# Optimization experiments

Measured on AMD Instinct MI355X. Metric: run time of the kernel, lower is better.

Reference implementation:

```python
import jax, jax.numpy as jnp
import numpy as np

N_NODES = 65536
NUM_GRAPHS = 128
NODES_PER_GRAPH = N_NODES // NUM_GRAPHS
HIDDEN = 512
EPS = 1e-6


def setup_inputs() -> dict:
    key = jax.random.key(0)
    k1, = jax.random.split(key, 1)
    x = jax.random.normal(k1, (N_NODES, HIDDEN), dtype=jnp.float32)
    gnw = jnp.ones((HIDDEN,), dtype=jnp.float32)
    gnb = jnp.zeros((HIDDEN,), dtype=jnp.float32)
    msc = jnp.ones((HIDDEN,), dtype=jnp.float32)
    batch_num = jnp.full((NUM_GRAPHS,), NODES_PER_GRAPH, dtype=jnp.int64)
    return {"x": x, "gnw": gnw, "gnb": gnb, "msc": msc, "batch_num": batch_num}


def reference(x, gnw, gnb, msc, batch_num):
    # x: [N, D] node features; batch_num: [B] per-graph node counts (sum == N)
    B = batch_num.shape[0]
    N = x.shape[0]
    seg = jnp.repeat(jnp.arange(B), batch_num, total_repeat_length=N)  # [N] graph id per node
    counts = batch_num.astype(x.dtype)[:, None]  # [B, 1]
    # per-graph mean: scatter-add then divide by segment size
    mean = jax.ops.segment_sum(x, seg, num_segments=B) / counts  # [B, D]
    sub = x - mean[seg] * msc  # [N, D]
    # per-graph variance of `sub` (matches original: second scatter_add of sub^2)
    var = jax.ops.segment_sum(sub * sub, seg, num_segments=B) / counts  # [B, D]
    std = jnp.sqrt(var + EPS)  # [B, D]
    return gnw * sub / std[seg] + gnb
```

## Files before the change

### kernel.cpp

```cpp
#include <hip/hip_runtime.h>


constexpr int N_NODES    = 65536;
constexpr int NUM_GRAPHS = 128;
constexpr int NPG        = N_NODES / NUM_GRAPHS;
constexpr int D          = 512;
constexpr int D4         = D / 4;
constexpr int RG         = 8;
constexpr int ROWS_PER_T = NPG / RG;
constexpr float EPS      = 1e-6f;

__global__ __launch_bounds__(1024) void k_graphnorm(const float* __restrict__ x,
                                                    const float* __restrict__ gnw,
                                                    const float* __restrict__ gnb,
                                                    const float* __restrict__ msc,
                                                    float* __restrict__ out) {
    __shared__ float4 lsum[RG][D4];
    __shared__ float4 lsq [RG][D4];
    __shared__ float4 lA[D4], lB[D4];

    const int g   = blockIdx.x;
    const int tid = threadIdx.x;
    const int cq  = tid & (D4 - 1);
    const int rg  = tid >> 7;

    const float4* xg = reinterpret_cast<const float4*>(x) + (size_t)g * NPG * D4;
    float4*       og = reinterpret_cast<float4*>(out)     + (size_t)g * NPG * D4;

    float4 s = make_float4(0.f, 0.f, 0.f, 0.f);
    float4 q = make_float4(0.f, 0.f, 0.f, 0.f);
    #pragma unroll 8
    for (int i = 0; i < ROWS_PER_T; ++i) {
        const int r = rg + i * RG;
        float4 v = xg[(size_t)r * D4 + cq];
        s.x += v.x; s.y += v.y; s.z += v.z; s.w += v.w;
        q.x = fmaf(v.x, v.x, q.x);
        q.y = fmaf(v.y, v.y, q.y);
        q.z = fmaf(v.z, v.z, q.z);
        q.w = fmaf(v.w, v.w, q.w);
    }
    lsum[rg][cq] = s;
    lsq [rg][cq] = q;
    __syncthreads();

    if (tid < D4) {
        const int d = tid;
        float4 S1 = lsum[0][d], S2 = lsq[0][d];
        #pragma unroll
        for (int j = 1; j < RG; ++j) {
            float4 a = lsum[j][d], b = lsq[j][d];
            S1.x += a.x; S1.y += a.y; S1.z += a.z; S1.w += a.w;
            S2.x += b.x; S2.y += b.y; S2.z += b.z; S2.w += b.w;
        }
        const float inv_n = 1.0f / (float)NPG;
        const float4 w4 = reinterpret_cast<const float4*>(gnw)[d];
        const float4 b4 = reinterpret_cast<const float4*>(gnb)[d];
        const float4 m4 = reinterpret_cast<const float4*>(msc)[d];
        float4 A, B;
        {
            float m, c, var, rstd;
            m = S1.x * inv_n; c = m * m4.x;
            var = fmaxf(fmaf(c, c, fmaf(-2.f * c, m, S2.x * inv_n)), 0.f);
            rstd = rsqrtf(var + EPS); A.x = w4.x * rstd; B.x = fmaf(-A.x, c, b4.x);
            m = S1.y * inv_n; c = m * m4.y;
            var = fmaxf(fmaf(c, c, fmaf(-2.f * c, m, S2.y * inv_n)), 0.f);
            rstd = rsqrtf(var + EPS); A.y = w4.y * rstd; B.y = fmaf(-A.y, c, b4.y);
            m = S1.z * inv_n; c = m * m4.z;
            var = fmaxf(fmaf(c, c, fmaf(-2.f * c, m, S2.z * inv_n)), 0.f);
            rstd = rsqrtf(var + EPS); A.z = w4.z * rstd; B.z = fmaf(-A.z, c, b4.z);
            m = S1.w * inv_n; c = m * m4.w;
            var = fmaxf(fmaf(c, c, fmaf(-2.f * c, m, S2.w * inv_n)), 0.f);
            rstd = rsqrtf(var + EPS); A.w = w4.w * rstd; B.w = fmaf(-A.w, c, b4.w);
        }
        lA[d] = A;
        lB[d] = B;
    }
    __syncthreads();

    const float4 a = lA[cq];
    const float4 b = lB[cq];
    #pragma unroll 8
    for (int i = 0; i < ROWS_PER_T; ++i) {
        const size_t o = (size_t)(rg + i * RG) * D4 + cq;
        float4 v = xg[o];
        float4 r;
        r.x = fmaf(a.x, v.x, b.x);
        r.y = fmaf(a.y, v.y, b.y);
        r.z = fmaf(a.z, v.z, b.z);
        r.w = fmaf(a.w, v.w, b.w);
        og[o] = r;
    }
}

extern "C" void kernel_launch(void* const* d_in, const int* in_sizes, int n_in,
                              void* d_out, int out_size, void* d_ws, size_t ws_size,
                              hipStream_t stream) {
    const float* x   = (const float*)d_in[0];
    const float* gnw = (const float*)d_in[1];
    const float* gnb = (const float*)d_in[2];
    const float* msc = (const float*)d_in[3];
    float* out = (float*)d_out;

    k_graphnorm<<<NUM_GRAPHS, 1024, 0, stream>>>(x, gnw, gnb, msc, out);
}
```

Baseline: 253.1 us.

## Split graph norm into stats, finalize, and normalize kernels across more blocks

Replaces the single kernel, which ran one 1024-thread block per graph (128 blocks), with three kernels. A partial-stats kernel over 2048 blocks writes per-slice sums to workspace, a small finalize kernel reduces them into per-graph scale/shift, and a normalize kernel over 2048 blocks applies them with nontemporal stores. The aim is to fill all CUs, since 128 blocks underuse a 256-CU GPU. In exchange it adds two extra launches and a workspace round trip, and x is still read twice.

```diff
diff --git a/kernel.cpp b/kernel.cpp
--- a/kernel.cpp
+++ b/kernel.cpp
@@ -1,94 +1,112 @@
 #include <hip/hip_runtime.h>
 
 
-constexpr int N_NODES    = 65536;
+using f32x4 = __attribute__((ext_vector_type(4))) float;
+
 constexpr int NUM_GRAPHS = 128;
-constexpr int NPG        = N_NODES / NUM_GRAPHS;
+constexpr int NPG        = 512;
 constexpr int D          = 512;
 constexpr int D4         = D / 4;
-constexpr int RG         = 8;
-constexpr int ROWS_PER_T = NPG / RG;
+constexpr int SLICES     = 16;
+constexpr int ROWS_PS    = NPG / SLICES;
+constexpr int RG         = 2;
+constexpr int ROWS_PT    = ROWS_PS / RG;
 constexpr float EPS      = 1e-6f;
 
-__global__ __launch_bounds__(1024) void k_graphnorm(const float* __restrict__ x,
-                                                    const float* __restrict__ gnw,
-                                                    const float* __restrict__ gnb,
-                                                    const float* __restrict__ msc,
-                                                    float* __restrict__ out) {
-    __shared__ float4 lsum[RG][D4];
-    __shared__ float4 lsq [RG][D4];
-    __shared__ float4 lA[D4], lB[D4];
 
-    const int g   = blockIdx.x;
-    const int tid = threadIdx.x;
-    const int cq  = tid & (D4 - 1);
-    const int rg  = tid >> 7;
+__global__ __launch_bounds__(256) void k_stats(const float* __restrict__ x,
+                                               f32x4* __restrict__ part) {
+    const int b  = blockIdx.x;
+    const int cq = threadIdx.x & (D4 - 1);
+    const int rg = threadIdx.x >> 7;
 
-    const float4* xg = reinterpret_cast<const float4*>(x) + (size_t)g * NPG * D4;
-    float4*       og = reinterpret_cast<float4*>(out)     + (size_t)g * NPG * D4;
+    const f32x4* xp = reinterpret_cast<const f32x4*>(x)
+                    + (size_t)b * ROWS_PS * D4 + (size_t)rg * D4 + cq;
 
-    float4 s = make_float4(0.f, 0.f, 0.f, 0.f);
-    float4 q = make_float4(0.f, 0.f, 0.f, 0.f);
-    #pragma unroll 8
-    for (int i = 0; i < ROWS_PER_T; ++i) {
-        const int r = rg + i * RG;
-        float4 v = xg[(size_t)r * D4 + cq];
-        s.x += v.x; s.y += v.y; s.z += v.z; s.w += v.w;
-        q.x = fmaf(v.x, v.x, q.x);
-        q.y = fmaf(v.y, v.y, q.y);
-        q.z = fmaf(v.z, v.z, q.z);
-        q.w = fmaf(v.w, v.w, q.w);
+    f32x4 s = {0.f, 0.f, 0.f, 0.f};
+    f32x4 q = {0.f, 0.f, 0.f, 0.f};
+    #pragma unroll
+    for (int i = 0; i < ROWS_PT; ++i) {
+        f32x4 v = xp[(size_t)i * RG * D4];
+        s += v;
+        q += v * v;
     }
-    lsum[rg][cq] = s;
-    lsq [rg][cq] = q;
-    __syncthreads();
 
-    if (tid < D4) {
-        const int d = tid;
-        float4 S1 = lsum[0][d], S2 = lsq[0][d];
+    f32x4* p = part + (((size_t)b * RG + rg) * 2) * D4 + cq;
+    p[0]  = s;
+    p[D4] = q;
+}
+
+__device__ inline float2 finalize1(float s1, float s2, float w, float bi,
+                                   float ms) {
+    const float inv_n = 1.0f / (float)NPG;
+    const float m = s1 * inv_n;
+    const float c = m * ms;
+    float var = fmaxf(fmaf(c, c, fmaf(-2.f * c, m, s2 * inv_n)), 0.f);
+    const float r = rsqrtf(var + EPS);
+    const float A = w * r;
+    const float B = fmaf(-A, c, bi);
+    return make_float2(A, B);
+}
+
+__global__ __launch_bounds__(256) void k_finalize(const f32x4* __restrict__ part,
+                                                  const float* __restrict__ gnw,
+                                                  const float* __restrict__ gnb,
+                                                  const float* __restrict__ msc,
+                                                  f32x4* __restrict__ Aa,
+                                                  f32x4* __restrict__ Ba) {
+    const int idx = blockIdx.x * 256 + threadIdx.x;
+    const int g   = idx >> 7;
+    const int cq  = idx & (D4 - 1);
+
+    f32x4 S1 = {0.f, 0.f, 0.f, 0.f};
+    f32x4 S2 = {0.f, 0.f, 0.f, 0.f};
+    #pragma unroll
+    for (int sl = 0; sl < SLICES; ++sl) {
         #pragma unroll
-        for (int j = 1; j < RG; ++j) {
-            float4 a = lsum[j][d], b = lsq[j][d];
-            S1.x += a.x; S1.y += a.y; S1.z += a.z; S1.w += a.w;
-            S2.x += b.x; S2.y += b.y; S2.z += b.z; S2.w += b.w;
+        for (int rg = 0; rg < RG; ++rg) {
+            const f32x4* p = part
+                + (((size_t)(g * SLICES + sl) * RG + rg) * 2) * D4 + cq;
+            S1 += p[0];
+            S2 += p[D4];
         }
-        const float inv_n = 1.0f / (float)NPG;
-        const float4 w4 = reinterpret_cast<const float4*>(gnw)[d];
-        const float4 b4 = reinterpret_cast<const float4*>(gnb)[d];
-        const float4 m4 = reinterpret_cast<const float4*>(msc)[d];
-        float4 A, B;
-        {
-            float m, c, var, rstd;
-            m = S1.x * inv_n; c = m * m4.x;
-            var = fmaxf(fmaf(c, c, fmaf(-2.f * c, m, S2.x * inv_n)), 0.f);
-            rstd = rsqrtf(var + EPS); A.x = w4.x * rstd; B.x = fmaf(-A.x, c, b4.x);
-            m = S1.y * inv_n; c = m * m4.y;
-            var = fmaxf(fmaf(c, c, fmaf(-2.f * c, m, S2.y * inv_n)), 0.f);
-            rstd = rsqrtf(var + EPS); A.y = w4.y * rstd; B.y = fmaf(-A.y, c, b4.y);
-            m = S1.z * inv_n; c = m * m4.z;
-            var = fmaxf(fmaf(c, c, fmaf(-2.f * c, m, S2.z * inv_n)), 0.f);
-            rstd = rsqrtf(var + EPS); A.z = w4.z * rstd; B.z = fmaf(-A.z, c, b4.z);
-            m = S1.w * inv_n; c = m * m4.w;
-            var = fmaxf(fmaf(c, c, fmaf(-2.f * c, m, S2.w * inv_n)), 0.f);
-            rstd = rsqrtf(var + EPS); A.w = w4.w * rstd; B.w = fmaf(-A.w, c, b4.w);
-        }
-        lA[d] = A;
-        lB[d] = B;
     }
-    __syncthreads();
 
-    const float4 a = lA[cq];
-    const float4 b = lB[cq];
-    #pragma unroll 8
-    for (int i = 0; i < ROWS_PER_T; ++i) {
-        const size_t o = (size_t)(rg + i * RG) * D4 + cq;
-        float4 v = xg[o];
-        float4 r;
-        r.x = fmaf(a.x, v.x, b.x);
-        r.y = fmaf(a.y, v.y, b.y);
-        r.z = fmaf(a.z, v.z, b.z);
-        r.w = fmaf(a.w, v.w, b.w);
-        og[o] = r;
+    const f32x4 w4 = reinterpret_cast<const f32x4*>(gnw)[cq];
+    const f32x4 b4 = reinterpret_cast<const f32x4*>(gnb)[cq];
+    const f32x4 m4 = reinterpret_cast<const f32x4*>(msc)[cq];
+    f32x4 A, B;
+    float2 r;
+    r = finalize1(S1.x, S2.x, w4.x, b4.x, m4.x); A.x = r.x; B.x = r.y;
+    r = finalize1(S1.y, S2.y, w4.y, b4.y, m4.y); A.y = r.x; B.y = r.y;
+    r = finalize1(S1.z, S2.z, w4.z, b4.z, m4.z); A.z = r.x; B.z = r.y;
+    r = finalize1(S1.w, S2.w, w4.w, b4.w, m4.w); A.w = r.x; B.w = r.y;
+
+    Aa[(size_t)g * D4 + cq] = A;
+    Ba[(size_t)g * D4 + cq] = B;
+}
+
+__global__ __launch_bounds__(256) void k_norm(const float* __restrict__ x,
+                                              const f32x4* __restrict__ Aa,
+                                              const f32x4* __restrict__ Ba,
+                                              float* __restrict__ out) {
+    const int b  = blockIdx.x;
+    const int g  = b >> 4;
+    const int cq = threadIdx.x & (D4 - 1);
+    const int rg = threadIdx.x >> 7;
+
+    const f32x4 a  = Aa[(size_t)g * D4 + cq];
+    const f32x4 bb = Ba[(size_t)g * D4 + cq];
+
+    const size_t base = (size_t)b * ROWS_PS * D4 + (size_t)rg * D4 + cq;
+    const f32x4* xp = reinterpret_cast<const f32x4*>(x) + base;
+    f32x4*       op = reinterpret_cast<f32x4*>(out) + base;
+
+    #pragma unroll
+    for (int i = 0; i < ROWS_PT; ++i) {
+        f32x4 v = xp[(size_t)i * RG * D4];
+        f32x4 r = a * v + bb;
+        __builtin_nontemporal_store(r, &op[(size_t)i * RG * D4]);
     }
 }
 
@@ -101,5 +119,12 @@
     const float* msc = (const float*)d_in[3];
     float* out = (float*)d_out;
 
-    k_graphnorm<<<NUM_GRAPHS, 1024, 0, stream>>>(x, gnw, gnb, msc, out);
+    f32x4* part = (f32x4*)d_ws;
+    f32x4* Aa   = part + (size_t)NUM_GRAPHS * SLICES * RG * 2 * D4;
+    f32x4* Ba   = Aa + (size_t)NUM_GRAPHS * D4;
+
+    k_stats   <<<NUM_GRAPHS * SLICES, 256, 0, stream>>>(x, part);
+    k_finalize<<<(NUM_GRAPHS * D4) / 256, 256, 0, stream>>>(part, gnw, gnb,
+                                                            msc, Aa, Ba);
+    k_norm    <<<NUM_GRAPHS * SLICES, 256, 0, stream>>>(x, Aa, Ba, out);
 }
```

After: 265.4 us. +4.8%, slower.
